# Kernel tuning notes

Hardware: AMD Instinct MI355X
Metric: run time of the kernel (lower is better)

## Reference

```python
import jax, jax.numpy as jnp
import numpy as np

B, D, L = 4096, 128, 4
ALPHA = 1.0
SLOPE = 0.1  # LeakyReLU negative slope


def _leaky(h):
    return jnp.where(h > 0, h, SLOPE * h)


def _dleaky(h):
    return jnp.where(h > 0, 1.0, SLOPE).astype(h.dtype)


def setup_inputs() -> dict:
    key = jax.random.key(0)
    ks = jax.random.split(key, 7)
    scale = 0.5 / np.sqrt(D)  # keep residual roughly Lipschitz < 1
    x = jax.random.normal(ks[0], (B, D), jnp.float32)
    W1 = jax.random.normal(ks[1], (L, D, D), jnp.float32) * scale
    b1 = jax.random.normal(ks[2], (L, D), jnp.float32) * 0.01
    W2 = jax.random.normal(ks[3], (L, D, D), jnp.float32) * scale
    b2 = jax.random.normal(ks[4], (L, D), jnp.float32) * 0.01
    W3 = jax.random.normal(ks[5], (L, D, D), jnp.float32) * scale
    b3 = jax.random.normal(ks[6], (L, D), jnp.float32) * 0.01
    return {"x": x, "W1": W1, "b1": b1, "W2": W2, "b2": b2, "W3": W3, "b3": b3}


def reference(x, W1, b1, W2, b2, W3, b3):
    logdet = jnp.zeros(x.shape[0], x.dtype)
    for i in range(L):  # small fixed number of structurally distinct blocks
        w1, w2, w3 = W1[i], W2[i], W3[i]
        # --- block forward: x <- x + alpha * f(x) ---
        h1 = x @ w1.T + b1[i]
        h2 = _leaky(h1) @ w2.T + b2[i]
        f = _leaky(h2) @ w3.T + b3[i]
        x = x + ALPHA * f
        # --- log|det J_f| evaluated at the NEW x (as in the original code) ---
        g1 = x @ w1.T + b1[i]          # [B, D] pre-activation 1
        d1 = _dleaky(g1)
        g2 = _leaky(g1) @ w2.T + b2[i]  # [B, D] pre-activation 2
        d2 = _dleaky(g2)
        # J[b] = w3 @ diag(d2[b]) @ w2 @ diag(d1[b]) @ w1  -> [B, D, D]
        J = (w3[None, :, :] * d2[:, None, :]) @ w2
        J = (J * d1[:, None, :]) @ w1
        s = jnp.linalg.svd(J, compute_uv=False)  # [B, D] singular values
        logdet = logdet + jnp.sum(jnp.log(s), axis=-1)
    return x, logdet
```

## Files before the change

kernel.cpp:

```cpp
#include <hip/hip_runtime.h>

typedef __attribute__((ext_vector_type(8))) short short8;
typedef __attribute__((ext_vector_type(4))) float float4f;

#define PITCH 136
#define ROWS 32
#define LOG_SLOPE -2.302585092994046f
#define LN2 0.6931471805599453f
#define NBLK 140
#define LDS_BYTES 69760
#define WS_BIAS 4160
#define WS_WPLANES 8192
#define NWELEM 196608

__device__ __forceinline__ float bf2f(unsigned int u) {
    return __builtin_bit_cast(float, u << 16);
}
__device__ __forceinline__ unsigned short f2bf(float f) {
    unsigned int x = __builtin_bit_cast(unsigned int, f);
    x += 0x7fff + ((x >> 16) & 1);
    return (unsigned short)(x >> 16);
}
__device__ __forceinline__ float4f vmsub(float4f a, float s, float4f b) {
    a[0] -= s * b[0]; a[1] -= s * b[1]; a[2] -= s * b[2]; a[3] -= s * b[3];
    return a;
}

template<int ISF32>
__device__ __forceinline__ float ldv(const void* p, int i) {
    if (ISF32) return ((const float*)p)[i];
    return bf2f(((const unsigned short*)p)[i]);
}

__device__ __forceinline__ int detect_f32(const unsigned short* W1u, int lane) {
    unsigned int u = W1u[lane * 2];
    unsigned int e = (u >> 7) & 0xFF;
    int bad = (e < 64) || (e > 135);
    return __ballot(bad) != 0ull;
}

__device__ __forceinline__ float4f mfma16(short8 a, short8 b, float4f c) {
    return __builtin_amdgcn_mfma_f32_16x16x32_bf16(a, b, c, 0, 0, 0);
}

__device__ __forceinline__ void split8(float4f a, float4f b, short8& hi, short8& lo) {
#pragma unroll
    for (int j = 0; j < 4; ++j) {
        float v = a[j]; unsigned short h = f2bf(v);
        hi[j] = (short)h; lo[j] = (short)f2bf(v - bf2f(h));
        v = b[j]; h = f2bf(v);
        hi[4 + j] = (short)h; lo[4 + j] = (short)f2bf(v - bf2f(h));
    }
}

__global__ void k_prep(const void* __restrict__ W1, const void* __restrict__ W2,
                       const void* __restrict__ W3, const void* __restrict__ b1,
                       const void* __restrict__ b2, const void* __restrict__ b3,
                       float* __restrict__ ws) {
    const int tid = threadIdx.x, bid = blockIdx.x;
    const int isf32 = detect_f32((const unsigned short*)W1, tid & 63);
    unsigned short* whi = (unsigned short*)(ws + WS_WPLANES);
    unsigned short* wlo = whi + NWELEM;
    if (bid < 96) {
        int s = (bid * 256 + tid) * 8;
        int mat = s >> 14, off = s & 16383;
        int wsel = mat >> 2;
        const void* Wm = wsel == 0 ? W1 : (wsel == 1 ? W2 : W3);
        int src = (mat & 3) * 16384 + off;
        short8 hi, lo;
        if (isf32) {
            const float* p = (const float*)Wm + src;
            split8(*(const float4f*)p, *(const float4f*)(p + 4), hi, lo);
        } else {
            hi = *(const short8*)((const unsigned short*)Wm + src);
            lo = (short8){0, 0, 0, 0, 0, 0, 0, 0};
        }
        *(short8*)(whi + s) = hi;
        *(short8*)(wlo + s) = lo;
    } else {
        for (int e = tid; e < 1536; e += 256) {
            int bsel = e >> 9, idx = e & 511;
            const void* bp = bsel == 0 ? b1 : (bsel == 1 ? b2 : b3);
            ws[WS_BIAS + e] = isf32 ? ((const float*)bp)[idx]
                                    : bf2f(((const unsigned short*)bp)[idx]);
        }
        if (tid == 0) ((int*)ws)[0] = 0;
    }
}

struct W8 { short8 v[16]; };

__device__ __forceinline__ W8 loadW(const unsigned short* __restrict__ wh,
                                    const unsigned short* __restrict__ wl,
                                    int c0, int c1, int q) {
    W8 r;
#pragma unroll
    for (int kk = 0; kk < 4; ++kk) {
        const int kc = kk * 32 + q * 8;
        r.v[kk * 4 + 0] = *(const short8*)(wh + c0 * 128 + kc);
        r.v[kk * 4 + 1] = *(const short8*)(wh + c1 * 128 + kc);
        r.v[kk * 4 + 2] = *(const short8*)(wl + c0 * 128 + kc);
        r.v[kk * 4 + 3] = *(const short8*)(wl + c1 * 128 + kc);
    }
    return r;
}

template<int MODE>
__device__ __forceinline__ W8 matvec(const W8& w,
        const unsigned short* inh, const unsigned short* inl,
        unsigned short* outh, unsigned short* outl,
        const unsigned short* resh, const unsigned short* resl,
        const unsigned short* __restrict__ nwh, const unsigned short* __restrict__ nwl,
        const float* __restrict__ bias,
        int lane, int colb, int* cnt) {
    const int m = lane & 15, q = lane >> 4;
    const int c0 = colb + m, c1 = colb + 16 + m;
    float b0 = bias[c0], b1v = bias[c1];
    float4f acc[2][2];
#pragma unroll
    for (int rt = 0; rt < 2; ++rt) {
        acc[rt][0] = (float4f){b0, b0, b0, b0};
        acc[rt][1] = (float4f){b1v, b1v, b1v, b1v};
    }
    __syncthreads();
    W8 wn = loadW(nwh, nwl, c0, c1, q);
#pragma unroll
    for (int kk = 0; kk < 4; ++kk) {
        const int kc = kk * 32 + q * 8;
#pragma unroll
        for (int rt = 0; rt < 2; ++rt) {
            short8 xh = *(const short8*)(inh + (rt * 16 + m) * PITCH + kc);
            short8 xl = *(const short8*)(inl + (rt * 16 + m) * PITCH + kc);
            acc[rt][0] = mfma16(xh, w.v[kk * 4 + 0], acc[rt][0]);
            acc[rt][0] = mfma16(xl, w.v[kk * 4 + 0], acc[rt][0]);
            acc[rt][0] = mfma16(xh, w.v[kk * 4 + 2], acc[rt][0]);
            acc[rt][1] = mfma16(xh, w.v[kk * 4 + 1], acc[rt][1]);
            acc[rt][1] = mfma16(xl, w.v[kk * 4 + 1], acc[rt][1]);
            acc[rt][1] = mfma16(xh, w.v[kk * 4 + 3], acc[rt][1]);
        }
    }
    int c[2][4];
#pragma unroll
    for (int rt = 0; rt < 2; ++rt) {
#pragma unroll
        for (int r = 0; r < 4; ++r) {
            float v0 = acc[rt][0][r], v1 = acc[rt][1][r];
            int row = rt * 16 + q * 4 + r;
            int o0 = row * PITCH + c0, o1 = row * PITCH + c1;
            if (MODE == 1) {
                v0 += bf2f(resh[o0]) + bf2f(resl[o0]);
                v1 += bf2f(resh[o1]) + bf2f(resl[o1]);
            }
            if (MODE >= 2) c[rt][r] = (v0 <= 0.0f) + (v1 <= 0.0f);
            if (MODE == 0 || MODE == 2) {
                v0 = v0 > 0.0f ? v0 : 0.1f * v0;
                v1 = v1 > 0.0f ? v1 : 0.1f * v1;
            }
            if (MODE != 3) {
                unsigned short h0 = f2bf(v0);
                outh[o0] = h0; outl[o0] = f2bf(v0 - bf2f(h0));
                unsigned short h1 = f2bf(v1);
                outh[o1] = h1; outl[o1] = f2bf(v1 - bf2f(h1));
            }
        }
    }
    if (MODE >= 2) {
#pragma unroll
        for (int rt = 0; rt < 2; ++rt) {
#pragma unroll
            for (int r = 0; r < 4; ++r) {
                int cc = c[rt][r];
                cc += __shfl_xor(cc, 1);
                cc += __shfl_xor(cc, 2);
                cc += __shfl_xor(cc, 4);
                cc += __shfl_xor(cc, 8);
                if (m == 0) atomicAdd(&cnt[rt * 16 + q * 4 + r], cc);
            }
        }
    }
    return wn;
}

template<int ISF32>
__device__ __forceinline__ void fwd(int bid, int tid, int lane, char* ldsb,
                                    const void* x, const float* ws, void* out,
                                    float* wsw) {
    unsigned short* P = (unsigned short*)ldsb;
    unsigned short* Ah = P;
    unsigned short* Al = P + 1 * ROWS * PITCH;
    unsigned short* Bh = P + 2 * ROWS * PITCH;
    unsigned short* Bl = P + 3 * ROWS * PITCH;
    unsigned short* Th = P + 4 * ROWS * PITCH;
    unsigned short* Tl = P + 5 * ROWS * PITCH;
    unsigned short* Uh = P + 6 * ROWS * PITCH;
    unsigned short* Ul = P + 7 * ROWS * PITCH;
    int* cnt = (int*)(P + 8 * ROWS * PITCH);
    const unsigned short* whi = (const unsigned short*)(ws + WS_WPLANES);
    const unsigned short* wlo = whi + NWELEM;
    const float* bias = ws + WS_BIAS;
    const int r0 = bid * ROWS;
    const int m = lane & 15, q = lane >> 4;
    const int colb = (tid >> 6) * 32;
    const int c0 = colb + m, c1 = colb + 16 + m;
    W8 wcur = loadW(whi, wlo, c0, c1, q);
    for (int e = tid; e < ROWS * 128; e += 256) {
        int r = e >> 7, c = e & 127;
        float v = ldv<ISF32>(x, (r0 + r) * 128 + c);
        unsigned short h = f2bf(v);
        Ah[r * PITCH + c] = h;
        Al[r * PITCH + c] = f2bf(v - bf2f(h));
    }
    if (tid < ROWS) cnt[tid] = 0;
    unsigned short *curh = Ah, *curl = Al, *othh = Bh, *othl = Bl;
#pragma unroll 1
    for (int layer = 0; layer < 4; ++layer) {
        const unsigned short* w1h = whi + (0 + layer) * 16384;
        const unsigned short* w1l = wlo + (0 + layer) * 16384;
        const unsigned short* w2h = whi + (4 + layer) * 16384;
        const unsigned short* w2l = wlo + (4 + layer) * 16384;
        const unsigned short* w3h = whi + (8 + layer) * 16384;
        const unsigned short* w3l = wlo + (8 + layer) * 16384;
        const unsigned short* n1h = whi + ((layer + 1) & 3) * 16384;
        const unsigned short* n1l = wlo + ((layer + 1) & 3) * 16384;
        const float* b1p = bias + layer * 128;
        const float* b2p = bias + 512 + layer * 128;
        const float* b3p = bias + 1024 + layer * 128;
        wcur = matvec<0>(wcur, curh, curl, Th, Tl, 0, 0, w2h, w2l, b1p, lane, colb, cnt);
        wcur = matvec<0>(wcur, Th, Tl, Uh, Ul, 0, 0, w3h, w3l, b2p, lane, colb, cnt);
        wcur = matvec<1>(wcur, Uh, Ul, othh, othl, curh, curl, w1h, w1l, b3p, lane, colb, cnt);
        wcur = matvec<2>(wcur, othh, othl, Th, Tl, 0, 0, w2h, w2l, b1p, lane, colb, cnt);
        wcur = matvec<3>(wcur, Th, Tl, Th, Tl, 0, 0, n1h, n1l, b2p, lane, colb, cnt);
        unsigned short* t;
        t = curh; curh = othh; othh = t;
        t = curl; curl = othl; othl = t;
    }
    __syncthreads();
    for (int e = tid; e < ROWS * 128; e += 256) {
        int r = e >> 7, c = e & 127;
        float v = bf2f(curh[r * PITCH + c]) + bf2f(curl[r * PITCH + c]);
        if (ISF32) ((float*)out)[(r0 + r) * 128 + c] = v;
        else ((unsigned short*)out)[(r0 + r) * 128 + c] = f2bf(v);
    }
    if (tid < ROWS) wsw[64 + r0 + tid] = (float)cnt[tid];
}

template<int ISF32>
__device__ __forceinline__ float lu_logdet(int id, int tid, float* lds,
        const void* W1, const void* W2, const void* W3) {
    const int wsel = id % 3;
    const void* Wm = (wsel == 0 ? W1 : (wsel == 1 ? W2 : W3));
    const int ofs = (id / 3) * 16384;
    const int tx = tid & 31, ty = tid >> 5;
    float* rowbuf = lds;
    float* colbuf = lds + 1024;
    float4f V[16];
#pragma unroll
    for (int m = 0; m < 16; ++m) {
        int base = ofs + (ty + 8 * m) * 128 + 4 * tx;
        if (ISF32) {
            V[m] = *(const float4f*)((const float*)Wm + base);
        } else {
            ushort4 u = *(const ushort4*)((const unsigned short*)Wm + base);
            V[m] = (float4f){bf2f(u.x), bf2f(u.y), bf2f(u.z), bf2f(u.w)};
        }
    }
    if (ty < 4) *(float4f*)&rowbuf[ty * 128 + 4 * tx] = V[0];
    if (tx == 0) {
#pragma unroll
        for (int j = 0; j < 4; ++j) {
#pragma unroll
            for (int mg = 0; mg < 4; ++mg) {
                float4f t = {V[mg * 4 + 0][j], V[mg * 4 + 1][j],
                             V[mg * 4 + 2][j], V[mg * 4 + 3][j]};
                *(float4f*)&colbuf[j * 128 + ty * 16 + mg * 4] = t;
            }
        }
    }
    __syncthreads();
    float logacc = 0.0f;
#pragma unroll 1
    for (int kap = 0; kap < 32; ++kap) {
        const int K = kap * 4;
        const int buf = (kap & 1) * 512;
        float4f D[4], R[4], C[4][4];
#pragma unroll
        for (int j = 0; j < 4; ++j) {
            D[j] = *(const float4f*)&rowbuf[buf + j * 128 + K];
            R[j] = *(const float4f*)&rowbuf[buf + j * 128 + 4 * tx];
#pragma unroll
            for (int mg = 0; mg < 4; ++mg)
                C[j][mg] = *(const float4f*)&colbuf[buf + j * 128 + ty * 16 + mg * 4];
        }
        float p0 = D[0][0], i0 = 1.0f / p0;
        float l10 = D[1][0] * i0, l20 = D[2][0] * i0, l30 = D[3][0] * i0;
        D[1] = vmsub(D[1], l10, D[0]); R[1] = vmsub(R[1], l10, R[0]);
        D[2] = vmsub(D[2], l20, D[0]); R[2] = vmsub(R[2], l20, R[0]);
        D[3] = vmsub(D[3], l30, D[0]); R[3] = vmsub(R[3], l30, R[0]);
        float p1 = D[1][1], i1 = 1.0f / p1;
        float l21 = D[2][1] * i1, l31 = D[3][1] * i1;
        D[2] = vmsub(D[2], l21, D[1]); R[2] = vmsub(R[2], l21, R[1]);
        D[3] = vmsub(D[3], l31, D[1]); R[3] = vmsub(R[3], l31, R[1]);
        float p2 = D[2][2], i2 = 1.0f / p2;
        float l32 = D[3][2] * i2;
        D[3] = vmsub(D[3], l32, D[2]); R[3] = vmsub(R[3], l32, R[2]);
        float p3 = D[3][3], i3 = 1.0f / p3;
        logacc += __log2f(fabsf(p0)) + __log2f(fabsf(p1))
                + __log2f(fabsf(p2)) + __log2f(fabsf(p3));
        float iv[4] = {i0, i1, i2, i3};
#pragma unroll
        for (int i = 0; i < 4; ++i) {
#pragma unroll
            for (int mg = 0; mg < 4; ++mg) {
#pragma unroll
                for (int e = 0; e < 4; ++e) {
                    int r = ty + 32 * mg + 8 * e;
                    C[i][mg][e] = (r > K + i) ? C[i][mg][e] * iv[i] : 0.0f;
                }
            }
#pragma unroll
            for (int j = i + 1; j < 4; ++j) {
                float uij = D[i][j];
#pragma unroll
                for (int mg = 0; mg < 4; ++mg)
                    C[j][mg] = vmsub(C[j][mg], uij, C[i][mg]);
            }
        }
#pragma unroll
        for (int mg = 0; mg < 4; ++mg) {
#pragma unroll
            for (int e = 0; e < 4; ++e) {
                float4f v = V[mg * 4 + e];
                v = vmsub(v, C[0][mg][e], R[0]);
                v = vmsub(v, C[1][mg][e], R[1]);
                v = vmsub(v, C[2][mg][e], R[2]);
                v = vmsub(v, C[3][mg][e], R[3]);
                V[mg * 4 + e] = v;
            }
        }
        if (kap < 31) {
            const int nbuf = ((kap + 1) & 1) * 512;
            const int tb = (kap & 1) ? 0 : 4;
            const int mn = (kap + 1) >> 1;
            if (ty >= tb && ty < tb + 4) {
                float4f val;
                switch (mn) {
                case 0:  val = V[0];  break; case 1:  val = V[1];  break;
                case 2:  val = V[2];  break; case 3:  val = V[3];  break;
                case 4:  val = V[4];  break; case 5:  val = V[5];  break;
                case 6:  val = V[6];  break; case 7:  val = V[7];  break;
                case 8:  val = V[8];  break; case 9:  val = V[9];  break;
                case 10: val = V[10]; break; case 11: val = V[11]; break;
                case 12: val = V[12]; break; case 13: val = V[13]; break;
                case 14: val = V[14]; break; default: val = V[15]; break;
                }
                *(float4f*)&rowbuf[nbuf + (ty - tb) * 128 + 4 * tx] = val;
            }
            if (tx == kap + 1) {
#pragma unroll
                for (int j = 0; j < 4; ++j) {
#pragma unroll
                    for (int mg = 0; mg < 4; ++mg) {
                        float4f t = {V[mg * 4 + 0][j], V[mg * 4 + 1][j],
                                     V[mg * 4 + 2][j], V[mg * 4 + 3][j]};
                        *(float4f*)&colbuf[nbuf + j * 128 + ty * 16 + mg * 4] = t;
                    }
                }
            }
        }
        __syncthreads();
    }
    return logacc * LN2;
}

__global__ __launch_bounds__(256) void k_main(
        const void* __restrict__ x,
        const void* __restrict__ W1, const void* __restrict__ b1,
        const void* __restrict__ W2, const void* __restrict__ b2,
        const void* __restrict__ W3, const void* __restrict__ b3,
        void* __restrict__ out, float* __restrict__ ws) {
    extern __shared__ __align__(16) char ldsb[];
    __shared__ int s_last;
    const int tid = threadIdx.x;
    const int lane = tid & 63;
    const int isf32 = detect_f32((const unsigned short*)W1, lane);

    if (blockIdx.x < 12) {
        float ld = isf32 ? lu_logdet<1>(blockIdx.x, tid, (float*)ldsb, W1, W2, W3)
                         : lu_logdet<0>(blockIdx.x, tid, (float*)ldsb, W1, W2, W3);
        if (tid == 0) ws[2 + blockIdx.x] = ld;
    } else {
        const int bid = blockIdx.x - 12;
        if (isf32) fwd<1>(bid, tid, lane, ldsb, x, ws, out, ws);
        else       fwd<0>(bid, tid, lane, ldsb, x, ws, out, ws);
    }

    __threadfence();
    if (tid == 0) s_last = (atomicAdd((int*)ws, 1) == NBLK - 1);
    __syncthreads();
    if (!s_last) return;
    __threadfence();
    float s = 0.0f;
#pragma unroll
    for (int i = 0; i < 12; ++i) s += ws[2 + i];
    for (int b = tid; b < 4096; b += 256) {
        float v = s + LOG_SLOPE * ws[64 + b];
        if (isf32) ((float*)out)[524288 + b] = v;
        else ((unsigned short*)out)[524288 + b] = f2bf(v);
    }
}

extern "C" void kernel_launch(void* const* d_in, const int* in_sizes, int n_in,
                              void* d_out, int out_size, void* d_ws, size_t ws_size,
                              hipStream_t stream) {
    const void* x  = d_in[0];
    const void* W1 = d_in[1];
    const void* b1 = d_in[2];
    const void* W2 = d_in[3];
    const void* b2 = d_in[4];
    const void* W3 = d_in[5];
    const void* b3 = d_in[6];
    float* ws = (float*)d_ws;

    hipLaunchKernelGGL(k_prep, dim3(97), dim3(256), 0, stream,
                       W1, W2, W3, b1, b2, b3, ws);
    hipLaunchKernelGGL(k_main, dim3(NBLK), dim3(256), LDS_BYTES, stream,
                       x, W1, b1, W2, b2, W3, b3, d_out, ws);
}
```

Baseline: 136.5 us.

## Fuse weight prep into main kernel with spin-wait flag instead of separate launch

Moves the weight split/bias conversion work into extra blocks of the main kernel. Forward blocks stage their inputs into LDS, then spin on a global counter until all prep blocks have signalled before loading weights. A memset resets the counters. This removes one kernel launch and the serialization between the two kernels. It relies on all blocks being co-resident to avoid deadlock, since 237 blocks with ~70KB LDS must fit at once. The LU log accumulation is also split into two accumulators to shorten a dependency chain.

```diff
diff --git a/kernel.cpp b/kernel.cpp
--- a/kernel.cpp
+++ b/kernel.cpp
@@ -7,7 +7,8 @@
 #define ROWS 32
 #define LOG_SLOPE -2.302585092994046f
 #define LN2 0.6931471805599453f
-#define NBLK 140
+#define NPREP 97
+#define NBLK 237
 #define LDS_BYTES 69760
 #define WS_BIAS 4160
 #define WS_WPLANES 8192
@@ -53,22 +54,20 @@
     }
 }
 
-__global__ void k_prep(const void* __restrict__ W1, const void* __restrict__ W2,
-                       const void* __restrict__ W3, const void* __restrict__ b1,
-                       const void* __restrict__ b2, const void* __restrict__ b3,
-                       float* __restrict__ ws) {
-    const int tid = threadIdx.x, bid = blockIdx.x;
-    const int isf32 = detect_f32((const unsigned short*)W1, tid & 63);
+template<int ISF32>
+__device__ __forceinline__ void prep(int pid, int tid,
+        const void* W1, const void* W2, const void* W3,
+        const void* b1, const void* b2, const void* b3, float* ws) {
     unsigned short* whi = (unsigned short*)(ws + WS_WPLANES);
     unsigned short* wlo = whi + NWELEM;
-    if (bid < 96) {
-        int s = (bid * 256 + tid) * 8;
+    if (pid < 96) {
+        int s = (pid * 256 + tid) * 8;
         int mat = s >> 14, off = s & 16383;
         int wsel = mat >> 2;
         const void* Wm = wsel == 0 ? W1 : (wsel == 1 ? W2 : W3);
         int src = (mat & 3) * 16384 + off;
         short8 hi, lo;
-        if (isf32) {
+        if (ISF32) {
             const float* p = (const float*)Wm + src;
             split8(*(const float4f*)p, *(const float4f*)(p + 4), hi, lo);
         } else {
@@ -81,11 +80,12 @@
         for (int e = tid; e < 1536; e += 256) {
             int bsel = e >> 9, idx = e & 511;
             const void* bp = bsel == 0 ? b1 : (bsel == 1 ? b2 : b3);
-            ws[WS_BIAS + e] = isf32 ? ((const float*)bp)[idx]
-                                    : bf2f(((const unsigned short*)bp)[idx]);
-        }
-        if (tid == 0) ((int*)ws)[0] = 0;
-    }
+            ws[WS_BIAS + e] = ldv<ISF32>(bp, idx);
+        }
+    }
+    __syncthreads();
+    __threadfence();
+    if (tid == 0) atomicAdd((int*)ws + 1, 1);
 }
 
 struct W8 { short8 v[16]; };
@@ -183,8 +183,7 @@
 
 template<int ISF32>
 __device__ __forceinline__ void fwd(int bid, int tid, int lane, char* ldsb,
-                                    const void* x, const float* ws, void* out,
-                                    float* wsw) {
+                                    const void* x, float* ws, void* out) {
     unsigned short* P = (unsigned short*)ldsb;
     unsigned short* Ah = P;
     unsigned short* Al = P + 1 * ROWS * PITCH;
@@ -202,7 +201,6 @@
     const int m = lane & 15, q = lane >> 4;
     const int colb = (tid >> 6) * 32;
     const int c0 = colb + m, c1 = colb + 16 + m;
-    W8 wcur = loadW(whi, wlo, c0, c1, q);
     for (int e = tid; e < ROWS * 128; e += 256) {
         int r = e >> 7, c = e & 127;
         float v = ldv<ISF32>(x, (r0 + r) * 128 + c);
@@ -211,6 +209,12 @@
         Al[r * PITCH + c] = f2bf(v - bf2f(h));
     }
     if (tid < ROWS) cnt[tid] = 0;
+    if (tid == 0) {
+        while (atomicAdd((int*)ws + 1, 0) < NPREP) {}
+    }
+    __syncthreads();
+    __threadfence();
+    W8 wcur = loadW(whi, wlo, c0, c1, q);
     unsigned short *curh = Ah, *curl = Al, *othh = Bh, *othl = Bl;
 #pragma unroll 1
     for (int layer = 0; layer < 4; ++layer) {
@@ -241,7 +245,7 @@
         if (ISF32) ((float*)out)[(r0 + r) * 128 + c] = v;
         else ((unsigned short*)out)[(r0 + r) * 128 + c] = f2bf(v);
     }
-    if (tid < ROWS) wsw[64 + r0 + tid] = (float)cnt[tid];
+    if (tid < ROWS) ws[64 + r0 + tid] = (float)cnt[tid];
 }
 
 template<int ISF32>
@@ -277,7 +281,7 @@
         }
     }
     __syncthreads();
-    float logacc = 0.0f;
+    float la0 = 0.0f, la1 = 0.0f;
 #pragma unroll 1
     for (int kap = 0; kap < 32; ++kap) {
         const int K = kap * 4;
@@ -304,8 +308,8 @@
         float l32 = D[3][2] * i2;
         D[3] = vmsub(D[3], l32, D[2]); R[3] = vmsub(R[3], l32, R[2]);
         float p3 = D[3][3], i3 = 1.0f / p3;
-        logacc += __log2f(fabsf(p0)) + __log2f(fabsf(p1))
-                + __log2f(fabsf(p2)) + __log2f(fabsf(p3));
+        la0 += __log2f(fabsf(p0)) + __log2f(fabsf(p1));
+        la1 += __log2f(fabsf(p2)) + __log2f(fabsf(p3));
         float iv[4] = {i0, i1, i2, i3};
 #pragma unroll
         for (int i = 0; i < 4; ++i) {
@@ -369,7 +373,7 @@
         }
         __syncthreads();
     }
-    return logacc * LN2;
+    return (la0 + la1) * LN2;
 }
 
 __global__ __launch_bounds__(256) void k_main(
@@ -388,10 +392,14 @@
         float ld = isf32 ? lu_logdet<1>(blockIdx.x, tid, (float*)ldsb, W1, W2, W3)
                          : lu_logdet<0>(blockIdx.x, tid, (float*)ldsb, W1, W2, W3);
         if (tid == 0) ws[2 + blockIdx.x] = ld;
+    } else if (blockIdx.x < 12 + NPREP) {
+        const int pid = blockIdx.x - 12;
+        if (isf32) prep<1>(pid, tid, W1, W2, W3, b1, b2, b3, ws);
+        else       prep<0>(pid, tid, W1, W2, W3, b1, b2, b3, ws);
     } else {
-        const int bid = blockIdx.x - 12;
-        if (isf32) fwd<1>(bid, tid, lane, ldsb, x, ws, out, ws);
-        else       fwd<0>(bid, tid, lane, ldsb, x, ws, out, ws);
+        const int bid = blockIdx.x - 12 - NPREP;
+        if (isf32) fwd<1>(bid, tid, lane, ldsb, x, ws, out);
+        else       fwd<0>(bid, tid, lane, ldsb, x, ws, out);
     }
 
     __threadfence();
@@ -421,8 +429,7 @@
     const void* b3 = d_in[6];
     float* ws = (float*)d_ws;
 
-    hipLaunchKernelGGL(k_prep, dim3(97), dim3(256), 0, stream,
-                       W1, W2, W3, b1, b2, b3, ws);
+    hipMemsetAsync(d_ws, 0, 8, stream);
     hipLaunchKernelGGL(k_main, dim3(NBLK), dim3(256), LDS_BYTES, stream,
                        x, W1, b1, W2, b2, W3, b3, d_out, ws);
 }
```

New measurement: 168.8 us. +23.6%, slower.

## Overlap trailing LU update with next panel read via lookahead

Applied to the files above, without the earlier changes.

Restructures the blocked LU logdet loop so that only the next panel's row and column values get the rank-4 update before they are written to LDS. The full trailing-matrix update is deferred until after the barrier and interleaved with the next panel's LDS reads, taking it off the critical path between barriers. The log accumulation is also split into two partial sums. This costs extra registers (copies of C and R) and some duplicated arithmetic for the panel values, which may reduce occupancy or cause spills.

```diff
diff --git a/kernel.cpp b/kernel.cpp
--- a/kernel.cpp
+++ b/kernel.cpp
@@ -277,20 +277,22 @@
         }
     }
     __syncthreads();
-    float logacc = 0.0f;
+    float4f D[4], R[4], C[4][4];
+    auto readPanel = [&](int bufb, int Kc) {
+#pragma unroll
+        for (int j = 0; j < 4; ++j) {
+            D[j] = *(const float4f*)&rowbuf[bufb + j * 128 + Kc];
+            R[j] = *(const float4f*)&rowbuf[bufb + j * 128 + 4 * tx];
+#pragma unroll
+            for (int mg = 0; mg < 4; ++mg)
+                C[j][mg] = *(const float4f*)&colbuf[bufb + j * 128 + ty * 16 + mg * 4];
+        }
+    };
+    readPanel(0, 0);
+    float la0 = 0.0f, la1 = 0.0f;
 #pragma unroll 1
     for (int kap = 0; kap < 32; ++kap) {
         const int K = kap * 4;
-        const int buf = (kap & 1) * 512;
-        float4f D[4], R[4], C[4][4];
-#pragma unroll
-        for (int j = 0; j < 4; ++j) {
-            D[j] = *(const float4f*)&rowbuf[buf + j * 128 + K];
-            R[j] = *(const float4f*)&rowbuf[buf + j * 128 + 4 * tx];
-#pragma unroll
-            for (int mg = 0; mg < 4; ++mg)
-                C[j][mg] = *(const float4f*)&colbuf[buf + j * 128 + ty * 16 + mg * 4];
-        }
         float p0 = D[0][0], i0 = 1.0f / p0;
         float l10 = D[1][0] * i0, l20 = D[2][0] * i0, l30 = D[3][0] * i0;
         D[1] = vmsub(D[1], l10, D[0]); R[1] = vmsub(R[1], l10, R[0]);
@@ -304,8 +306,8 @@
         float l32 = D[3][2] * i2;
         D[3] = vmsub(D[3], l32, D[2]); R[3] = vmsub(R[3], l32, R[2]);
         float p3 = D[3][3], i3 = 1.0f / p3;
-        logacc += __log2f(fabsf(p0)) + __log2f(fabsf(p1))
-                + __log2f(fabsf(p2)) + __log2f(fabsf(p3));
+        la0 += __log2f(fabsf(p0)) + __log2f(fabsf(p1));
+        la1 += __log2f(fabsf(p2)) + __log2f(fabsf(p3));
         float iv[4] = {i0, i1, i2, i3};
 #pragma unroll
         for (int i = 0; i < 4; ++i) {
@@ -323,18 +325,6 @@
 #pragma unroll
                 for (int mg = 0; mg < 4; ++mg)
                     C[j][mg] = vmsub(C[j][mg], uij, C[i][mg]);
-            }
-        }
-#pragma unroll
-        for (int mg = 0; mg < 4; ++mg) {
-#pragma unroll
-            for (int e = 0; e < 4; ++e) {
-                float4f v = V[mg * 4 + e];
-                v = vmsub(v, C[0][mg][e], R[0]);
-                v = vmsub(v, C[1][mg][e], R[1]);
-                v = vmsub(v, C[2][mg][e], R[2]);
-                v = vmsub(v, C[3][mg][e], R[3]);
-                V[mg * 4 + e] = v;
             }
         }
         if (kap < 31) {
@@ -342,34 +332,71 @@
             const int tb = (kap & 1) ? 0 : 4;
             const int mn = (kap + 1) >> 1;
             if (ty >= tb && ty < tb + 4) {
-                float4f val;
+                float4f val; float g0, g1, g2, g3;
                 switch (mn) {
-                case 0:  val = V[0];  break; case 1:  val = V[1];  break;
-                case 2:  val = V[2];  break; case 3:  val = V[3];  break;
-                case 4:  val = V[4];  break; case 5:  val = V[5];  break;
-                case 6:  val = V[6];  break; case 7:  val = V[7];  break;
-                case 8:  val = V[8];  break; case 9:  val = V[9];  break;
-                case 10: val = V[10]; break; case 11: val = V[11]; break;
-                case 12: val = V[12]; break; case 13: val = V[13]; break;
-                case 14: val = V[14]; break; default: val = V[15]; break;
+                case 0:  val = V[0];  g0=C[0][0][0]; g1=C[1][0][0]; g2=C[2][0][0]; g3=C[3][0][0]; break;
+                case 1:  val = V[1];  g0=C[0][0][1]; g1=C[1][0][1]; g2=C[2][0][1]; g3=C[3][0][1]; break;
+                case 2:  val = V[2];  g0=C[0][0][2]; g1=C[1][0][2]; g2=C[2][0][2]; g3=C[3][0][2]; break;
+                case 3:  val = V[3];  g0=C[0][0][3]; g1=C[1][0][3]; g2=C[2][0][3]; g3=C[3][0][3]; break;
+                case 4:  val = V[4];  g0=C[0][1][0]; g1=C[1][1][0]; g2=C[2][1][0]; g3=C[3][1][0]; break;
+                case 5:  val = V[5];  g0=C[0][1][1]; g1=C[1][1][1]; g2=C[2][1][1]; g3=C[3][1][1]; break;
+                case 6:  val = V[6];  g0=C[0][1][2]; g1=C[1][1][2]; g2=C[2][1][2]; g3=C[3][1][2]; break;
+                case 7:  val = V[7];  g0=C[0][1][3]; g1=C[1][1][3]; g2=C[2][1][3]; g3=C[3][1][3]; break;
+                case 8:  val = V[8];  g0=C[0][2][0]; g1=C[1][2][0]; g2=C[2][2][0]; g3=C[3][2][0]; break;
+                case 9:  val = V[9];  g0=C[0][2][1]; g1=C[1][2][1]; g2=C[2][2][1]; g3=C[3][2][1]; break;
+                case 10: val = V[10]; g0=C[0][2][2]; g1=C[1][2][2]; g2=C[2][2][2]; g3=C[3][2][2]; break;
+                case 11: val = V[11]; g0=C[0][2][3]; g1=C[1][2][3]; g2=C[2][2][3]; g3=C[3][2][3]; break;
+                case 12: val = V[12]; g0=C[0][3][0]; g1=C[1][3][0]; g2=C[2][3][0]; g3=C[3][3][0]; break;
+                case 13: val = V[13]; g0=C[0][3][1]; g1=C[1][3][1]; g2=C[2][3][1]; g3=C[3][3][1]; break;
+                case 14: val = V[14]; g0=C[0][3][2]; g1=C[1][3][2]; g2=C[2][3][2]; g3=C[3][3][2]; break;
+                default: val = V[15]; g0=C[0][3][3]; g1=C[1][3][3]; g2=C[2][3][3]; g3=C[3][3][3]; break;
                 }
+                val = vmsub(val, g0, R[0]); val = vmsub(val, g1, R[1]);
+                val = vmsub(val, g2, R[2]); val = vmsub(val, g3, R[3]);
                 *(float4f*)&rowbuf[nbuf + (ty - tb) * 128 + 4 * tx] = val;
             }
             if (tx == kap + 1) {
 #pragma unroll
-                for (int j = 0; j < 4; ++j) {
+                for (int j0 = 0; j0 < 4; ++j0) {
 #pragma unroll
                     for (int mg = 0; mg < 4; ++mg) {
-                        float4f t = {V[mg * 4 + 0][j], V[mg * 4 + 1][j],
-                                     V[mg * 4 + 2][j], V[mg * 4 + 3][j]};
-                        *(float4f*)&colbuf[nbuf + j * 128 + ty * 16 + mg * 4] = t;
+                        float4f t;
+#pragma unroll
+                        for (int e = 0; e < 4; ++e) {
+                            t[e] = V[mg * 4 + e][j0]
+                                 - (C[0][mg][e] * R[0][j0] + C[1][mg][e] * R[1][j0]
+                                  + C[2][mg][e] * R[2][j0] + C[3][mg][e] * R[3][j0]);
+                        }
+                        *(float4f*)&colbuf[nbuf + j0 * 128 + ty * 16 + mg * 4] = t;
                     }
                 }
             }
         }
         __syncthreads();
-    }
-    return logacc * LN2;
+        float4f Cb[4][4], Rb[4];
+#pragma unroll
+        for (int j = 0; j < 4; ++j) {
+            Rb[j] = R[j];
+#pragma unroll
+            for (int mg = 0; mg < 4; ++mg) Cb[j][mg] = C[j][mg];
+        }
+        if (kap < 31) {
+            readPanel(((kap + 1) & 1) * 512, K + 4);
+#pragma unroll
+            for (int mg = 0; mg < 4; ++mg) {
+#pragma unroll
+                for (int e = 0; e < 4; ++e) {
+                    float4f v = V[mg * 4 + e];
+                    v = vmsub(v, Cb[0][mg][e], Rb[0]);
+                    v = vmsub(v, Cb[1][mg][e], Rb[1]);
+                    v = vmsub(v, Cb[2][mg][e], Rb[2]);
+                    v = vmsub(v, Cb[3][mg][e], Rb[3]);
+                    V[mg * 4 + e] = v;
+                }
+            }
+        }
+    }
+    return (la0 + la1) * LN2;
 }
 
 __global__ __launch_bounds__(256) void k_main(
```

After: 162.8 us. +19.2%, slower.
